# Optimization experiments

Measured on AMD Instinct MI355X. Metric: run time of the kernel, lower is better.

The kernel has to match this reference:

```python
import jax, jax.numpy as jnp
import numpy as np

NUM_SUBSET = 3
BN_EPS = 1e-5
T_CONST = 40
NUM_HEADS = 8


def _unit_gcn(x, PA, Wa, ba, Wb, bb, Wd, bd, gamma, beta):
    # x: (B, C, T, V). 1x1 convs become channel einsums. flag=True, GMPool_G,
    # num_point not in {3,7} -> adjacency A = PA only. down = identity (C_in==C_out).
    B, C, T, V = x.shape
    inter = Wa.shape[1]
    x_flat = x.reshape(B, C * T, V)
    y = None
    for i in range(NUM_SUBSET):
        a = jnp.einsum('bctv,ic->bitv', x, Wa[i]) + ba[i][None, :, None, None]
        A1 = a.transpose(0, 3, 1, 2).reshape(B, V, inter * T)          # (B, V, inter*T)
        b = jnp.einsum('bctv,ic->bitv', x, Wb[i]) + bb[i][None, :, None, None]
        A2 = b.reshape(B, inter * T, V)                                 # (B, inter*T, V)
        S = jax.nn.softmax((A1 @ A2) / (inter * T), axis=-2) + PA[i]    # (B, V, V), Softmax(-2)
        z = (x_flat @ S).reshape(B, C, T, V)
        z = jnp.einsum('bctv,oc->botv', z, Wd[i]) + bd[i][None, :, None, None]
        y = z if y is None else y + z
    # BatchNorm2d (eval: running_mean=0, running_var=1)
    y = y * (gamma / jnp.sqrt(1.0 + BN_EPS))[None, :, None, None] + beta[None, :, None, None]
    y = y + x  # residual via identity down-path
    return jax.nn.relu(y)


def _mab_forward(Q, K, fck, fcv, fco):
    B, Npt, DK = K.shape
    T = T_CONST
    C = DK // T
    Kr = K.transpose(0, 2, 1).reshape(B, C, T, Npt)   # (B, C, T, V)
    Kg = _unit_gcn(Kr, *fck)
    Vg = _unit_gcn(Kr, *fcv)
    Kf = Kg.transpose(0, 3, 1, 2).reshape(B, Npt, -1)  # (B, V, C*T)
    Vf = Vg.transpose(0, 3, 1, 2).reshape(B, Npt, -1)
    S, DV = Q.shape[1], Q.shape[2]
    ds = DV // NUM_HEADS
    Qh = Q.reshape(B, S, NUM_HEADS, ds)
    Kh = Kf.reshape(B, Npt, NUM_HEADS, ds)
    Vh = Vf.reshape(B, Npt, NUM_HEADS, ds)
    scores = jnp.einsum('bqhd,bkhd->bhqk', Qh, Kh) / jnp.sqrt(jnp.float32(DV))
    attn = jax.nn.softmax(scores, axis=-1)  # softmax_dim=2 of (H*B, S, V) == last axis
    Oh = Qh + jnp.einsum('bhqk,bkhd->bqhd', attn, Vh)
    O = Oh.reshape(B, S, DV)  # cat over heads along feature dim == reshape
    Og = O.transpose(0, 2, 1).reshape(B, C, T, S)
    Og = _unit_gcn(Og, *fco)
    Og = Og.transpose(0, 3, 1, 2).reshape(B, S, -1)
    return O + jax.nn.relu(Og)


def setup_inputs() -> dict:
    key = jax.random.key(0)
    ks = jax.random.split(key, 8)
    B, Npt, Sd, T, C, inter = 256, 25, 10, 40, 64, 16
    D = C * T  # 2560

    def gcn_params(kk, V):
        k = jax.random.split(kk, 5)
        return dict(
            PA=jnp.full((3, V, V), 1e-6, jnp.float32),
            Wa=jax.random.normal(k[0], (3, inter, C), jnp.float32) * np.float32(np.sqrt(2.0 / C)),
            ba=jnp.zeros((3, inter), jnp.float32),
            Wb=jax.random.normal(k[1], (3, inter, C), jnp.float32) * np.float32(np.sqrt(2.0 / C)),
            bb=jnp.zeros((3, inter), jnp.float32),
            Wd=jax.random.normal(k[2], (3, C, C), jnp.float32) * np.float32(np.sqrt(2.0 / (3 * C))),
            bd=jnp.zeros((3, C), jnp.float32),
            gamma=jax.random.uniform(k[3], (C,), jnp.float32, 0.5, 1.5),
            beta=jax.random.normal(k[4], (C,), jnp.float32) * 0.01,
        )

    inp = {
        'Q': jax.random.normal(ks[0], (B, Sd, D), jnp.float32),
        'K': jax.random.normal(ks[1], (B, Npt, D), jnp.float32),
    }
    for pref, kk, V in (('fck', ks[2], Npt), ('fcv', ks[3], Npt), ('fco', ks[4], Sd)):
        for n, v in gcn_params(kk, V).items():
            inp[pref + '_' + n] = v
    for n in ('relrec_s1', 'relsend_s1', 'relrec_s2', 'relsend_s2', 'relrec_speed', 'relsend_speed'):
        inp[n] = jnp.zeros((1,), jnp.int32)  # unused (branch only active for V==7, T==20)
    return inp


def reference(Q, K,
              fck_PA, fck_Wa, fck_ba, fck_Wb, fck_bb, fck_Wd, fck_bd, fck_gamma, fck_beta,
              fcv_PA, fcv_Wa, fcv_ba, fcv_Wb, fcv_bb, fcv_Wd, fcv_bd, fcv_gamma, fcv_beta,
              fco_PA, fco_Wa, fco_ba, fco_Wb, fco_bb, fco_Wd, fco_bd, fco_gamma, fco_beta,
              relrec_s1, relsend_s1, relrec_s2, relsend_s2, relrec_speed, relsend_speed):
    fck = (fck_PA, fck_Wa, fck_ba, fck_Wb, fck_bb, fck_Wd, fck_bd, fck_gamma, fck_beta)
    fcv = (fcv_PA, fcv_Wa, fcv_ba, fcv_Wb, fcv_bb, fcv_Wd, fcv_bd, fcv_gamma, fcv_beta)
    fco = (fco_PA, fco_Wa, fco_ba, fco_Wb, fco_bb, fco_Wd, fco_bd, fco_gamma, fco_beta)
    return _mab_forward(Q, K, fck, fcv, fco)
```

## Files before the change

### kernel.cpp

```cpp
#include <hip/hip_runtime.h>
#include <hip/hip_bf16.h>

#define BB 256
#define CC 64
#define TT 40
#define DD 2560
#define V1 25
#define V2 10
#define INTER 16
#define NH 8
#define DSH 320
#define HSLAB 8000

typedef __hip_bfloat16 bf16;
typedef unsigned int uint;
typedef unsigned short ushort;
typedef __attribute__((ext_vector_type(8))) short bf16x8;
typedef __attribute__((ext_vector_type(4))) float f32x4;

__device__ __forceinline__ float b2f(bf16 x) { return __bfloat162float(x); }

__device__ __forceinline__ ushort f2bb(float f) {
    uint x = __float_as_uint(f);
    uint r = x + 0x7fffu + ((x >> 16) & 1u);
    return (ushort)(r >> 16);
}
__device__ __forceinline__ float blo(uint u) { return __uint_as_float(u << 16); }
__device__ __forceinline__ float bhi(uint u) { return __uint_as_float(u & 0xffff0000u); }
__device__ __forceinline__ float b2f_us(ushort h) { return __uint_as_float(((uint)h) << 16); }
__device__ __forceinline__ uint4 pack8(const float* a) {
    uint4 pk;
    pk.x = (uint)f2bb(a[0]) | ((uint)f2bb(a[1]) << 16);
    pk.y = (uint)f2bb(a[2]) | ((uint)f2bb(a[3]) << 16);
    pk.z = (uint)f2bb(a[4]) | ((uint)f2bb(a[5]) << 16);
    pk.w = (uint)f2bb(a[6]) | ((uint)f2bb(a[7]) << 16);
    return pk;
}

__device__ __forceinline__ int swz64(int row, int col) {
    return row * 64 + ((((col >> 3) ^ row) & 7) << 3) + (col & 7);
}
__device__ __forceinline__ int swzC(int c, int col) {
    return c * 128 + ((((col >> 3) ^ c) & 15) << 3) + (col & 7);
}
__device__ __forceinline__ int swz320(int row, int k) {
    const int g = k >> 3;
    return row * 320 + (((g & ~7) | ((g ^ row) & 7)) << 3) + (k & 7);
}

__global__ __launch_bounds__(256) void prep_wabf(
    const float* __restrict__ Wa0, const float* __restrict__ Wb0,
    const float* __restrict__ Wa1, const float* __restrict__ Wb1,
    ushort* __restrict__ Wabf) {
    const int tid = threadIdx.x;
    for (int e = tid; e < 768; e += 256) {
        const int lane = e & 63, mat = (e >> 6) & 3, s = e >> 8;
        const int ln = lane & 15, lq = lane >> 4;
        const float* Wp = (mat == 0) ? Wa0 : (mat == 1) ? Wb0 : (mat == 2) ? Wa1 : Wb1;
        const float* src = Wp + s * 1024 + ln * 64 + lq * 8;
        ushort* dst = Wabf + e * 16;
        #pragma unroll
        for (int i = 0; i < 8; ++i) {
            dst[i] = f2bb(src[i]);
            dst[8 + i] = f2bb(src[32 + i]);
        }
    }
}

__global__ __launch_bounds__(512) void gcn_S3(
    const float* __restrict__ X,
    const ushort* __restrict__ Wabf,
    const float* __restrict__ ba0, const float* __restrict__ bb0,
    const float* __restrict__ ba1, const float* __restrict__ bb1,
    bf16* __restrict__ Xw, float* __restrict__ Mpart) {
    __shared__ ushort xsT[208][72];
    __shared__ ushort abT[4][32][136];
    __shared__ float biasS3[192];

    const int tid = threadIdx.x;
    const int b = blockIdx.x & 255, tc = blockIdx.x >> 8;
    const int t0 = tc * 8;
    const int lane = tid & 63, w = tid >> 6;
    const int ln = lane & 15, lq = lane >> 4;
    const int mat = w & 3, half = w >> 2;

    const float* Xb = X + (size_t)b * V1 * DD;
    for (int e = tid; e < V1 * 64; e += 512) {
        const int v = e >> 6, c = e & 63;
        const float* src = Xb + (size_t)v * DD + c * TT + t0;
        const float4 f0 = *(const float4*)src;
        const float4 f1 = *(const float4*)(src + 4);
        const float tmp[8] = {f0.x, f0.y, f0.z, f0.w, f1.x, f1.y, f1.z, f1.w};
        #pragma unroll
        for (int tl = 0; tl < 8; ++tl) xsT[v * 8 + tl][c] = f2bb(tmp[tl]);
    }
    if (tid < 192) {
        const int s = tid >> 6, m2 = (tid >> 4) & 3, j = tid & 15;
        const float* bp = (m2 == 0) ? ba0 : (m2 == 1) ? bb0 : (m2 == 2) ? ba1 : bb1;
        biasS3[tid] = bp[s * 16 + j];
    }
    __syncthreads();

    for (int e = tid; e < 1600; e += 512) {
        const int v = e >> 6, h = (e >> 3) & 7, tl = e & 7;
        *(uint4*)(Xw + (size_t)(b * NH + h) * HSLAB + v * 320 + (t0 + tl) * 8) =
            *(const uint4*)&xsT[v * 8 + tl][h * 8];
    }

    for (int s = 0; s < 3; ++s) {
        const ushort* wp = Wabf + (((s * 4 + mat) * 64 + lane) << 4);
        union { uint4 u; bf16x8 v; } ua, ub;
        ua.u = *(const uint4*)wp;
        ub.u = *(const uint4*)(wp + 8);
        float br[4];
        #pragma unroll
        for (int r = 0; r < 4; ++r) br[r] = biasS3[s * 64 + mat * 16 + lq * 4 + r];

        if (s) __syncthreads();

        const int ntEnd = half ? 13 : 7;
        for (int nt = half ? 7 : 0; nt < ntEnd; ++nt) {
            const bf16x8 b0 = *(const bf16x8*)&xsT[nt * 16 + ln][lq * 8];
            const bf16x8 b1 = *(const bf16x8*)&xsT[nt * 16 + ln][lq * 8 + 32];
            f32x4 acc = (f32x4){0.f, 0.f, 0.f, 0.f};
            acc = __builtin_amdgcn_mfma_f32_16x16x32_bf16(ua.v, b0, acc, 0, 0, 0);
            acc = __builtin_amdgcn_mfma_f32_16x16x32_bf16(ub.v, b1, acc, 0, 0, 0);
            const int p = nt * 16 + ln;
            if (p < 200) {
                const int v = p >> 3, tl = p & 7;
                #pragma unroll
                for (int r = 0; r < 4; ++r)
                    abT[mat][v][(lq * 4 + r) * 8 + tl] = f2bb(acc[r] + br[r]);
            }
        }
        __syncthreads();

        {
            const int np = w >> 2, mt = (w >> 1) & 1, ntl = w & 1;
            const ushort* Ap = &abT[np * 2 + 0][mt * 16 + ln][lq * 8];
            const ushort* Bp = &abT[np * 2 + 1][ntl * 16 + ln][lq * 8];
            f32x4 g = (f32x4){0.f, 0.f, 0.f, 0.f};
            g = __builtin_amdgcn_mfma_f32_16x16x32_bf16(
                    *(const bf16x8*)Ap, *(const bf16x8*)Bp, g, 0, 0, 0);
            g = __builtin_amdgcn_mfma_f32_16x16x32_bf16(
                    *(const bf16x8*)(Ap + 32), *(const bf16x8*)(Bp + 32), g, 0, 0, 0);
            g = __builtin_amdgcn_mfma_f32_16x16x32_bf16(
                    *(const bf16x8*)(Ap + 64), *(const bf16x8*)(Bp + 64), g, 0, 0, 0);
            g = __builtin_amdgcn_mfma_f32_16x16x32_bf16(
                    *(const bf16x8*)(Ap + 96), *(const bf16x8*)(Bp + 96), g, 0, 0, 0);
            const int vp = ntl * 16 + ln;
            if (vp < V1) {
                float* Mb = Mpart + (((size_t)tc * 256 + b) * 6 + (s * 2 + np)) * 625;
                #pragma unroll
                for (int r = 0; r < 4; ++r) {
                    const int v = mt * 16 + lq * 4 + r;
                    if (v < V1) Mb[v * V1 + vp] = g[r];
                }
            }
        }
    }
}

__global__ __launch_bounds__(128) void reduce_softmax(
    const float* __restrict__ Mpart,
    const float* __restrict__ PA0, const float* __restrict__ PA1,
    const float* __restrict__ WdK, const float* __restrict__ WdV,
    ushort* __restrict__ Sbf, ushort* __restrict__ Wdf) {
    __shared__ float Ms[625];
    const int tid = threadIdx.x, b = blockIdx.x, snp = blockIdx.y;
    const int s = snp >> 1, np = snp & 1;

    if (b == 0) {
        for (int e = tid; e < 256; e += 128) {
            const int wv = e >> 6, l = e & 63;
            const int lnn = l & 15, lqq = l >> 4;
            const float* Wp = (np ? WdV : WdK) + s * 4096 + (wv * 16 + lnn) * 64 + lqq * 8;
            ushort* dst = Wdf + (((np * 3 + s) * 4 + wv) * 64 + l) * 16;
            #pragma unroll
            for (int j = 0; j < 8; ++j) {
                dst[j] = f2bb(Wp[j]);
                dst[8 + j] = f2bb(Wp[32 + j]);
            }
        }
    }

    for (int e = tid; e < 625; e += 128) {
        float sum = 0.f;
        #pragma unroll
        for (int tcc = 0; tcc < 5; ++tcc)
            sum += Mpart[(((size_t)tcc * 256 + b) * 6 + snp) * 625 + e];
        Ms[e] = sum;
    }
    __syncthreads();
    if (tid < 32) {
        ushort* SbfRow = Sbf + ((((size_t)b * 2 + np) * 3 + s) << 10) + tid * 32;
        if (tid < V1) {
            const int vp = tid;
            const float invIT = 1.0f / 640.0f;
            float mx = -1e30f;
            for (int v = 0; v < V1; ++v) mx = fmaxf(mx, Ms[v * V1 + vp]);
            float sum = 0.f;
            for (int v = 0; v < V1; ++v) sum += expf((Ms[v * V1 + vp] - mx) * invIT);
            const float rs = 1.f / sum;
            const float* PAn = np ? PA1 : PA0;
            for (int v = 0; v < V1; ++v) {
                const float e_ = expf((Ms[v * V1 + vp] - mx) * invIT);
                SbfRow[v] = f2bb(e_ * rs + PAn[(s * V1 + v) * V1 + vp]);
            }
            for (int v = V1; v < 32; ++v) SbfRow[v] = 0;
        } else {
            for (int v = 0; v < 32; ++v) SbfRow[v] = 0;
        }
    }
}

__global__ __launch_bounds__(256) void gcn_S2O(
    const float* __restrict__ X,
    const float* __restrict__ Wa0, const float* __restrict__ ba0,
    const float* __restrict__ Wb0, const float* __restrict__ bb0,
    const float* __restrict__ PA0, const float* __restrict__ WdO,
    ushort* __restrict__ SbfO, ushort* __restrict__ Wdf3) {
    constexpr int V = V2;
    constexpr int P = 80;
    __shared__ ushort xs[64][P];
    __shared__ ushort ab[32][P];
    __shared__ ushort wT[64][32];
    __shared__ float biasL[32];
    __shared__ float M[100];

    const int tid = threadIdx.x, b = blockIdx.x, s = blockIdx.y;

    if (b == 0) {
        const int e = tid;
        if (e < 256) {
            const int wv = e >> 6, l = e & 63;
            const int lnn = l & 15, lqq = l >> 4;
            const float* Wp = WdO + s * 4096 + (wv * 16 + lnn) * 64 + lqq * 8;
            ushort* dst = Wdf3 + (((s * 4 + wv) * 64 + l) << 4);
            #pragma unroll
            for (int j = 0; j < 8; ++j) {
                dst[j] = f2bb(Wp[j]);
                dst[8 + j] = f2bb(Wp[32 + j]);
            }
        }
    }

    for (int e = tid; e < 16 * 64; e += 256) {
        int c = e & 63, j = e >> 6;
        wT[c][j]      = f2bb(Wa0[s * 1024 + e]);
        wT[c][16 + j] = f2bb(Wb0[s * 1024 + e]);
    }
    if (tid < 16) {
        biasL[tid]      = ba0[s * 16 + tid];
        biasL[16 + tid] = bb0[s * 16 + tid];
    }

    float macc = 0.f;

    const float* Xb = X + (size_t)b * V * DD;
    for (int tc = 0; tc < 5; ++tc) {
        const int t0 = tc * 8;
        for (int e = tid; e < V * 64; e += 256) {
            const int v = e >> 6, c = e & 63;
            const float* src = Xb + (size_t)v * DD + c * TT + t0;
            const float4 f0 = *(const float4*)src;
            const float4 f1 = *(const float4*)(src + 4);
            const float tmp[8] = {f0.x, f0.y, f0.z, f0.w, f1.x, f1.y, f1.z, f1.w};
            *(uint4*)&xs[c][v * 8] = pack8(tmp);
        }
        __syncthreads();
        for (int tau = tid; tau < 80; tau += 256) {
            const int rq = tau % 8, co = tau / 8;
            float acc[4][8];
            #pragma unroll
            for (int r = 0; r < 4; ++r) {
                const float bv = biasL[4 * rq + r];
                #pragma unroll
                for (int cc = 0; cc < 8; ++cc) acc[r][cc] = bv;
            }
            for (int c = 0; c < 64; ++c) {
                const uint2 wv = *(const uint2*)&wT[c][4 * rq];
                const uint4 xv = *(const uint4*)&xs[c][8 * co];
                const float w0 = blo(wv.x), w1 = bhi(wv.x);
                const float w2 = blo(wv.y), w3 = bhi(wv.y);
                const float x0 = blo(xv.x), x1 = bhi(xv.x);
                const float x2 = blo(xv.y), x3 = bhi(xv.y);
                const float x4 = blo(xv.z), x5 = bhi(xv.z);
                const float x6 = blo(xv.w), x7 = bhi(xv.w);
                acc[0][0] += w0 * x0; acc[0][1] += w0 * x1;
                acc[0][2] += w0 * x2; acc[0][3] += w0 * x3;
                acc[0][4] += w0 * x4; acc[0][5] += w0 * x5;
                acc[0][6] += w0 * x6; acc[0][7] += w0 * x7;
                acc[1][0] += w1 * x0; acc[1][1] += w1 * x1;
                acc[1][2] += w1 * x2; acc[1][3] += w1 * x3;
                acc[1][4] += w1 * x4; acc[1][5] += w1 * x5;
                acc[1][6] += w1 * x6; acc[1][7] += w1 * x7;
                acc[2][0] += w2 * x0; acc[2][1] += w2 * x1;
                acc[2][2] += w2 * x2; acc[2][3] += w2 * x3;
                acc[2][4] += w2 * x4; acc[2][5] += w2 * x5;
                acc[2][6] += w2 * x6; acc[2][7] += w2 * x7;
                acc[3][0] += w3 * x0; acc[3][1] += w3 * x1;
                acc[3][2] += w3 * x2; acc[3][3] += w3 * x3;
                acc[3][4] += w3 * x4; acc[3][5] += w3 * x5;
                acc[3][6] += w3 * x6; acc[3][7] += w3 * x7;
            }
            #pragma unroll
            for (int r = 0; r < 4; ++r)
                *(uint4*)&ab[4 * rq + r][8 * co] = pack8(acc[r]);
        }
        __syncthreads();
        if (tid < 100) {
            const int v = tid / V, vp = tid % V;
            float mm = 0.f;
            #pragma unroll
            for (int j = 0; j < 16; ++j) {
                const uint4 av = *(const uint4*)&ab[j][v * 8];
                const uint4 bv = *(const uint4*)&ab[16 + j][vp * 8];
                mm += blo(av.x) * blo(bv.x) + bhi(av.x) * bhi(bv.x)
                    + blo(av.y) * blo(bv.y) + bhi(av.y) * bhi(bv.y)
                    + blo(av.z) * blo(bv.z) + bhi(av.z) * bhi(bv.z)
                    + blo(av.w) * blo(bv.w) + bhi(av.w) * bhi(bv.w);
            }
            macc += mm;
        }
    }

    if (tid < 100) M[tid] = macc;
    __syncthreads();

    const float invIT = 1.0f / 640.0f;
    if (tid < 16) {
        ushort* So = SbfO + ((size_t)b * 3 + s) * 256 + tid * 16;
        if (tid < V) {
            const int vp = tid;
            float mx = -1e30f;
            for (int v = 0; v < V; ++v) mx = fmaxf(mx, M[v * V + vp]);
            float sum = 0.f;
            for (int v = 0; v < V; ++v) sum += expf((M[v * V + vp] - mx) * invIT);
            const float rs = 1.f / sum;
            for (int v = 0; v < V; ++v) {
                const float e_ = expf((M[v * V + vp] - mx) * invIT);
                So[v] = f2bb(e_ * rs + PA0[(s * V + v) * V + vp]);
            }
            for (int v = V; v < 16; ++v) So[v] = 0;
        } else {
            for (int v = 0; v < 16; ++v) So[v] = 0;
        }
    }
}

__global__ __launch_bounds__(256) void gcn_applyKV(
    const bf16* __restrict__ Xbf,
    const ushort* __restrict__ Sbf, const ushort* __restrict__ Wdf,
    const float* __restrict__ bdK, const float* __restrict__ gK, const float* __restrict__ beK,
    const float* __restrict__ bdV, const float* __restrict__ gV, const float* __restrict__ beV,
    bf16* __restrict__ Kg, bf16* __restrict__ Vg) {

    __shared__ ushort xsT[100 * 64];
    __shared__ ushort SlTs[6144];
    __shared__ ushort uC[8192];
    __shared__ float bias6[6 * 64];

    const int tid = threadIdx.x, b = blockIdx.x, chunk = blockIdx.y;
    const int lane = tid & 63, w = tid >> 6;
    const int ln = lane & 15, lq = lane >> 4;
    const int t0 = chunk * 4;

    if (tid < 64) {
        bias6[tid]       = bdK[tid] + bdK[64 + tid] + bdK[128 + tid];
        bias6[64 + tid]  = bdV[tid] + bdV[64 + tid] + bdV[128 + tid];
        bias6[128 + tid] = gK[tid] * rsqrtf(1.f + 1e-5f);
        bias6[192 + tid] = gV[tid] * rsqrtf(1.f + 1e-5f);
        bias6[256 + tid] = beK[tid];
        bias6[320 + tid] = beV[tid];
    }
    const bf16* Xb = Xbf + (size_t)b * NH * HSLAB;
    for (int e = tid; e < 1024; e += 256) {
        const int h = e >> 7, v = (e >> 2) & 31, tl = e & 3;
        if (v < V1)
            *(uint4*)&xsT[swz64(v * 4 + tl, h * 8)] =
                *(const uint4*)(Xb + (size_t)h * HSLAB + v * 320 + (t0 + tl) * 8);
    }
    {
        const ushort* Sb = Sbf + (size_t)b * 6144;
        for (int e = tid; e < 768; e += 256)
            ((uint4*)SlTs)[e] = ((const uint4*)Sb)[e];
    }
    __syncthreads();

    {
        const int c = lane, q = w;
        #pragma unroll
        for (int j = 0; j < 4; ++j) {
            ushort vals[8];
            #pragma unroll
            for (int i = 0; i < 8; ++i) {
                const int v0 = q * 8 + i;
                vals[i] = (v0 < V1) ? xsT[swz64(v0 * 4 + j, c)] : (ushort)0;
            }
            uint4 pk;
            pk.x = (uint)vals[0] | ((uint)vals[1] << 16);
            pk.y = (uint)vals[2] | ((uint)vals[3] << 16);
            pk.z = (uint)vals[4] | ((uint)vals[5] << 16);
            pk.w = (uint)vals[6] | ((uint)vals[7] << 16);
            *(uint4*)&uC[swzC(c, j * 32 + q * 8)] = pk;
        }
    }
    __syncthreads();

    bf16x8 aF[4];
    #pragma unroll
    for (int tl = 0; tl < 4; ++tl)
        aF[tl] = *(const bf16x8*)&uC[swzC(w * 16 + ln, tl * 32 + lq * 8)];
    __syncthreads();

    for (int g = 0; g < 2; ++g) {
        f32x4 acc[7];
        #pragma unroll
        for (int tn = 0; tn < 7; ++tn) acc[tn] = (f32x4){0.f, 0.f, 0.f, 0.f};

        for (int s = 0; s < 3; ++s) {
            const ushort* wp = Wdf + ((((g * 3 + s) * 4 + w) * 64 + lane) << 4);
            union { uint4 u; bf16x8 v; } ua, ub;
            ua.u = *(const uint4*)wp;
            ub.u = *(const uint4*)(wp + 8);

            if (g | s) __syncthreads();

            #pragma unroll
            for (int nt = 0; nt < 2; ++nt) {
                const bf16x8 bF =
                    *(const bf16x8*)&SlTs[((g * 3 + s) << 10) + (nt * 16 + ln) * 32 + lq * 8];
                const int v = nt * 16 + ln;
                #pragma unroll
                for (int tl = 0; tl < 4; ++tl) {
                    f32x4 d = (f32x4){0.f, 0.f, 0.f, 0.f};
                    d = __builtin_amdgcn_mfma_f32_16x16x32_bf16(aF[tl], bF, d, 0, 0, 0);
                    if (v < V1) {
                        uint2 pk;
                        pk.x = (uint)f2bb(d[0]) | ((uint)f2bb(d[1]) << 16);
                        pk.y = (uint)f2bb(d[2]) | ((uint)f2bb(d[3]) << 16);
                        *(uint2*)&uC[swz64(v * 4 + tl, w * 16 + lq * 4)] = pk;
                    }
                }
            }
            __syncthreads();

            #pragma unroll
            for (int tn = 0; tn < 7; ++tn) {
                const bf16x8 b0 = *(const bf16x8*)&uC[swz64(tn * 16 + ln, lq * 8)];
                const bf16x8 b1 = *(const bf16x8*)&uC[swz64(tn * 16 + ln, lq * 8 + 32)];
                acc[tn] = __builtin_amdgcn_mfma_f32_16x16x32_bf16(ua.v, b0, acc[tn], 0, 0, 0);
                acc[tn] = __builtin_amdgcn_mfma_f32_16x16x32_bf16(ub.v, b1, acc[tn], 0, 0, 0);
            }
        }
        __syncthreads();

        {
            const int c0 = w * 16 + lq * 4;
            float bb[4], ss[4], be[4];
            #pragma unroll
            for (int r = 0; r < 4; ++r) {
                bb[r] = bias6[g * 64 + c0 + r];
                ss[r] = bias6[128 + g * 64 + c0 + r];
                be[r] = bias6[256 + g * 64 + c0 + r];
            }
            #pragma unroll
            for (int tn = 0; tn < 7; ++tn) {
                const int p = tn * 16 + ln;
                if (p < 100) {
                    const uint2 u = *(const uint2*)&xsT[swz64(p, c0)];
                    const float rs[4] = {blo(u.x), bhi(u.x), blo(u.y), bhi(u.y)};
                    float y[4];
                    #pragma unroll
                    for (int r = 0; r < 4; ++r)
                        y[r] = fmaxf((acc[tn][r] + bb[r]) * ss[r] + be[r] + rs[r], 0.f);
                    uint2 pk;
                    pk.x = (uint)f2bb(y[0]) | ((uint)f2bb(y[1]) << 16);
                    pk.y = (uint)f2bb(y[2]) | ((uint)f2bb(y[3]) << 16);
                    *(uint2*)&uC[swz64(p, c0)] = pk;
                }
            }
        }
        __syncthreads();

        bf16* outp = (g ? Vg : Kg) + (size_t)b * NH * HSLAB;
        for (int e = tid; e < 1024; e += 256) {
            const int h = e >> 7, v = (e >> 2) & 31, tl = e & 3;
            if (v < V1)
                *(uint4*)(outp + (size_t)h * HSLAB + v * 320 + (t0 + tl) * 8) =
                    *(const uint4*)&uC[swz64(v * 4 + tl, h * 8)];
        }
    }
}

__global__ __launch_bounds__(256) void gcn_applyO(
    const float* __restrict__ X,
    const ushort* __restrict__ SbfO, const ushort* __restrict__ Wdf3,
    const float* __restrict__ bdO, const float* __restrict__ gO, const float* __restrict__ beO,
    float* __restrict__ out_f, const float* __restrict__ Obuf) {

    __shared__ ushort xsT[80 * 64];
    __shared__ ushort uC[8192];
    __shared__ ushort SlTs16[832];
    __shared__ float bias3[3 * 64];

    const int tid = threadIdx.x, b = blockIdx.x, chunk = blockIdx.y;
    const int lane = tid & 63, w = tid >> 6;
    const int ln = lane & 15, lq = lane >> 4;
    const int t0 = chunk * 8;

    if (tid < 64) {
        bias3[tid]       = bdO[tid] + bdO[64 + tid] + bdO[128 + tid];
        bias3[64 + tid]  = gO[tid] * rsqrtf(1.f + 1e-5f);
        bias3[128 + tid] = beO[tid];
    }
    const float* Xb = X + (size_t)b * V2 * DD;
    for (int e = tid; e < 640; e += 256) {
        const int v = e >> 6, c = e & 63;
        const float* src = Xb + (size_t)v * DD + c * TT + t0;
        const float4 f0 = *(const float4*)src;
        const float4 f1 = *(const float4*)(src + 4);
        const float tmp[8] = {f0.x, f0.y, f0.z, f0.w, f1.x, f1.y, f1.z, f1.w};
        #pragma unroll
        for (int tl = 0; tl < 8; ++tl) xsT[swz64(v * 8 + tl, c)] = f2bb(tmp[tl]);
    }
    {
        const uint4* Sb = (const uint4*)(SbfO + (size_t)b * 768);
        for (int e = tid; e < 96; e += 256) ((uint4*)SlTs16)[e] = Sb[e];
    }
    __syncthreads();

    {
        const int c = lane;
        #pragma unroll
        for (int jj = 0; jj < 4; ++jj) {
            const int u_ = w * 4 + jj;
            const int tl = u_ >> 1, q = u_ & 1;
            ushort vals[8];
            #pragma unroll
            for (int i = 0; i < 8; ++i) {
                const int v0 = q * 8 + i;
                vals[i] = (v0 < V2) ? xsT[swz64(v0 * 8 + tl, c)] : (ushort)0;
            }
            uint4 pk;
            pk.x = (uint)vals[0] | ((uint)vals[1] << 16);
            pk.y = (uint)vals[2] | ((uint)vals[3] << 16);
            pk.z = (uint)vals[4] | ((uint)vals[5] << 16);
            pk.w = (uint)vals[6] | ((uint)vals[7] << 16);
            *(uint4*)&uC[swzC(c, tl * 16 + q * 8)] = pk;
        }
    }
    __syncthreads();

    union { uint4 u; bf16x8 v; } z8; z8.u = (uint4){0u, 0u, 0u, 0u};
    bf16x8 aF[8];
    #pragma unroll
    for (int tl = 0; tl < 8; ++tl)
        aF[tl] = (lq < 2) ? *(const bf16x8*)&uC[swzC(w * 16 + ln, tl * 16 + lq * 8)]
                          : z8.v;
    __syncthreads();

    f32x4 acc[5];
    #pragma unroll
    for (int tn = 0; tn < 5; ++tn) acc[tn] = (f32x4){0.f, 0.f, 0.f, 0.f};

    for (int s = 0; s < 3; ++s) {
        const ushort* wp = Wdf3 + (((s * 4 + w) * 64 + lane) << 4);
        union { uint4 u; bf16x8 v; } ua, ub;
        ua.u = *(const uint4*)wp;
        ub.u = *(const uint4*)(wp + 8);

        if (s) __syncthreads();

        const bf16x8 bF = (lq < 2)
            ? *(const bf16x8*)&SlTs16[s * 256 + ln * 16 + lq * 8] : z8.v;
        #pragma unroll
        for (int tl = 0; tl < 8; ++tl) {
            f32x4 d = (f32x4){0.f, 0.f, 0.f, 0.f};
            d = __builtin_amdgcn_mfma_f32_16x16x32_bf16(aF[tl], bF, d, 0, 0, 0);
            if (ln < V2) {
                uint2 pk;
                pk.x = (uint)f2bb(d[0]) | ((uint)f2bb(d[1]) << 16);
                pk.y = (uint)f2bb(d[2]) | ((uint)f2bb(d[3]) << 16);
                *(uint2*)&uC[swz64(ln * 8 + tl, w * 16 + lq * 4)] = pk;
            }
        }
        __syncthreads();

        #pragma unroll
        for (int tn = 0; tn < 5; ++tn) {
            const bf16x8 b0 = *(const bf16x8*)&uC[swz64(tn * 16 + ln, lq * 8)];
            const bf16x8 b1 = *(const bf16x8*)&uC[swz64(tn * 16 + ln, lq * 8 + 32)];
            acc[tn] = __builtin_amdgcn_mfma_f32_16x16x32_bf16(ua.v, b0, acc[tn], 0, 0, 0);
            acc[tn] = __builtin_amdgcn_mfma_f32_16x16x32_bf16(ub.v, b1, acc[tn], 0, 0, 0);
        }
    }
    __syncthreads();

    {
        const int c0 = w * 16 + lq * 4;
        float bb[4], ss[4], be[4];
        #pragma unroll
        for (int r = 0; r < 4; ++r) {
            bb[r] = bias3[c0 + r];
            ss[r] = bias3[64 + c0 + r];
            be[r] = bias3[128 + c0 + r];
        }
        #pragma unroll
        for (int tn = 0; tn < 5; ++tn) {
            const int p = tn * 16 + ln;
            const uint2 u = *(const uint2*)&xsT[swz64(p, c0)];
            const float rs[4] = {blo(u.x), bhi(u.x), blo(u.y), bhi(u.y)};
            float y[4];
            #pragma unroll
            for (int r = 0; r < 4; ++r)
                y[r] = fmaxf((acc[tn][r] + bb[r]) * ss[r] + be[r] + rs[r], 0.f);
            uint2 pk;
            pk.x = (uint)f2bb(y[0]) | ((uint)f2bb(y[1]) << 16);
            pk.y = (uint)f2bb(y[2]) | ((uint)f2bb(y[3]) << 16);
            *(uint2*)&uC[swz64(p, c0)] = pk;
        }
    }
    __syncthreads();

    {
        const int v = tid & 15, ci = tid >> 4;
        if (v < V2) {
            #pragma unroll
            for (int r = 0; r < 4; ++r) {
                const int c = ci * 4 + r;
                const size_t base = (size_t)b * V2 * DD + (size_t)v * DD + c * TT + t0;
                const float4 o0 = *(const float4*)&Obuf[base];
                const float4 o1 = *(const float4*)&Obuf[base + 4];
                float4 y0, y1;
                y0.x = o0.x + b2f_us(uC[swz64(v * 8 + 0, c)]);
                y0.y = o0.y + b2f_us(uC[swz64(v * 8 + 1, c)]);
                y0.z = o0.z + b2f_us(uC[swz64(v * 8 + 2, c)]);
                y0.w = o0.w + b2f_us(uC[swz64(v * 8 + 3, c)]);
                y1.x = o1.x + b2f_us(uC[swz64(v * 8 + 4, c)]);
                y1.y = o1.y + b2f_us(uC[swz64(v * 8 + 5, c)]);
                y1.z = o1.z + b2f_us(uC[swz64(v * 8 + 6, c)]);
                y1.w = o1.w + b2f_us(uC[swz64(v * 8 + 7, c)]);
                *(float4*)&out_f[base] = y0;
                *(float4*)&out_f[base + 4] = y1;
            }
        }
    }
}

__global__ __launch_bounds__(256) void attn_kernel(const float* __restrict__ Q,
                                                   const bf16* __restrict__ Kg,
                                                   const bf16* __restrict__ Vg,
                                                   float* __restrict__ O) {
    __shared__ float smA[10240];
    __shared__ float attP[4][16][16];
    __shared__ float attF[16][32];
    ushort* qs2h = (ushort*)smA;
    ushort* qs2l = (ushort*)smA + 5120;
    ushort* ksw  = (ushort*)smA + 10240;
    float* vbuf = smA;

    const int b = blockIdx.x, h = blockIdx.y, tid = threadIdx.x;
    const int lane = tid & 63, w = tid >> 6;
    const int ln = lane & 15, lq = lane >> 4;

    const float* Qb = Q + (size_t)b * 10 * DD + h * DSH;
    for (int e = tid; e < 800; e += 256) {
        const int q = e / 80, seg = e % 80;
        const int dd0 = seg * 4;
        const float4 f = *(const float4*)(Qb + (size_t)q * DD + dd0);
        const float ff[4] = {f.x, f.y, f.z, f.w};
        #pragma unroll
        for (int j = 0; j < 4; ++j) {
            const int dd = dd0 + j;
            const int k = (dd % 40) * 8 + dd / 40;
            const int idx = swz320(q, k);
            const ushort hi = f2bb(ff[j]);
            qs2h[idx] = hi;
            qs2l[idx] = f2bb(ff[j] - b2f_us(hi));
        }
    }
    const bf16* Kb = Kg + (size_t)(b * NH + h) * HSLAB;
    for (int e = tid; e < 1000; e += 256) {
        const int kk = e / 40, g = e % 40;
        const int gp = (g & ~7) | ((g ^ kk) & 7);
        *(uint4*)&ksw[kk * 320 + gp * 8] = *(const uint4*)(Kb + (size_t)e * 8);
    }
    __syncthreads();

    {
        const int ntl = w & 1;
        const int ch0 = (w >> 1) * 5;
        f32x4 d = (f32x4){0.f, 0.f, 0.f, 0.f};
        #pragma unroll
        for (int c5 = 0; c5 < 5; ++c5) {
            const int k0 = (ch0 + c5) * 32 + lq * 8;
            const bf16x8 ah = *(const bf16x8*)&qs2h[swz320(ln, k0)];
            const bf16x8 al = *(const bf16x8*)&qs2l[swz320(ln, k0)];
            const bf16x8 bF = *(const bf16x8*)&ksw[swz320(ntl * 16 + ln, k0)];
            d = __builtin_amdgcn_mfma_f32_16x16x32_bf16(ah, bF, d, 0, 0, 0);
            d = __builtin_amdgcn_mfma_f32_16x16x32_bf16(al, bF, d, 0, 0, 0);
        }
        #pragma unroll
        for (int r = 0; r < 4; ++r) attP[w][lq * 4 + r][ln] = d[r];
    }
    __syncthreads();

    const float scale = 0.019764235376052370f;
    for (int e = tid; e < 512; e += 256) {
        const int q = e >> 5, kk = e & 31;
        const int ntl = kk >> 4, kkl = kk & 15;
        attF[q][kk] = (attP[ntl][q][kkl] + attP[ntl + 2][q][kkl]) * scale;
    }
    const bf16* Vb = Vg + (size_t)(b * NH + h) * HSLAB;
    for (int e = tid; e < 1000; e += 256) {
        const int kk = e / TT, t = e % TT;
        const uint4 u = *(const uint4*)(Vb + (size_t)e * 8);
        const ushort* us = (const ushort*)&u;
        float* dst = &vbuf[kk * 324 + t];
        #pragma unroll
        for (int cl = 0; cl < 8; ++cl) dst[cl * 40] = b2f_us(us[cl]);
    }
    __syncthreads();

    if (tid < 10) {
        float mx = -1e30f;
        for (int k = 0; k < V1; ++k) mx = fmaxf(mx, attF[tid][k]);
        float sum = 0.f;
        for (int k = 0; k < V1; ++k) {
            float e_ = expf(attF[tid][k] - mx);
            attF[tid][k] = e_;
            sum += e_;
        }
        float r = 1.0f / sum;
        for (int k = 0; k < V1; ++k) attF[tid][k] *= r;
    }
    __syncthreads();

    float* Ob = O + (size_t)b * 10 * DD + h * DSH;
    for (int e = tid; e < 800; e += 256) {
        const int q = e / 80, seg = e % 80;
        const int dl0 = seg * 4;
        float ax = 0.f, ay = 0.f, az = 0.f, aw = 0.f;
        #pragma unroll
        for (int kk = 0; kk < V1; ++kk) {
            const float a = attF[q][kk];
            const float4 v = *(const float4*)&vbuf[kk * 324 + dl0];
            ax += a * v.x; ay += a * v.y; az += a * v.z; aw += a * v.w;
        }
        const float4 qv = *(const float4*)(Qb + (size_t)q * DD + dl0);
        float4 o;
        o.x = qv.x + ax; o.y = qv.y + ay; o.z = qv.z + az; o.w = qv.w + aw;
        *(float4*)(Ob + (size_t)q * DD + dl0) = o;
    }
}

extern "C" void kernel_launch(void* const* d_in, const int* in_sizes, int n_in,
                              void* d_out, int out_size, void* d_ws, size_t ws_size,
                              hipStream_t stream) {
    const float* Q = (const float*)d_in[0];
    const float* K = (const float*)d_in[1];
    const float* fck_PA = (const float*)d_in[2];
    const float* fck_Wa = (const float*)d_in[3];
    const float* fck_ba = (const float*)d_in[4];
    const float* fck_Wb = (const float*)d_in[5];
    const float* fck_bb = (const float*)d_in[6];
    const float* fck_Wd = (const float*)d_in[7];
    const float* fck_bd = (const float*)d_in[8];
    const float* fck_gamma = (const float*)d_in[9];
    const float* fck_beta = (const float*)d_in[10];
    const float* fcv_PA = (const float*)d_in[11];
    const float* fcv_Wa = (const float*)d_in[12];
    const float* fcv_ba = (const float*)d_in[13];
    const float* fcv_Wb = (const float*)d_in[14];
    const float* fcv_bb = (const float*)d_in[15];
    const float* fcv_Wd = (const float*)d_in[16];
    const float* fcv_bd = (const float*)d_in[17];
    const float* fcv_gamma = (const float*)d_in[18];
    const float* fcv_beta = (const float*)d_in[19];
    const float* fco_PA = (const float*)d_in[20];
    const float* fco_Wa = (const float*)d_in[21];
    const float* fco_ba = (const float*)d_in[22];
    const float* fco_Wb = (const float*)d_in[23];
    const float* fco_bb = (const float*)d_in[24];
    const float* fco_Wd = (const float*)d_in[25];
    const float* fco_bd = (const float*)d_in[26];
    const float* fco_gamma = (const float*)d_in[27];
    const float* fco_beta = (const float*)d_in[28];

    char* wsb = (char*)d_ws;
    bf16* Xbf = (bf16*)(wsb);
    bf16* Vg = (bf16*)(wsb);
    bf16* Kg = (bf16*)(wsb + 32768000);
    float* Mpart = (float*)(wsb + 65536000);
    float* O = (float*)(wsb + 65536000);
    ushort* Sbf = (ushort*)(wsb + 84736000);
    ushort* Wdf = (ushort*)(wsb + 88000000);
    ushort* SbfO = (ushort*)(wsb + 32768000);
    ushort* Wdf3 = (ushort*)(wsb + 33300000);
    ushort* Wabf = (ushort*)(wsb + 95590400);

    prep_wabf<<<dim3(1), dim3(256), 0, stream>>>(
        fck_Wa, fck_Wb, fcv_Wa, fcv_Wb, Wabf);

    gcn_S3<<<dim3(BB * 5), dim3(512), 0, stream>>>(
        K, Wabf, fck_ba, fck_bb, fcv_ba, fcv_bb, Xbf, Mpart);

    reduce_softmax<<<dim3(BB, 6), dim3(128), 0, stream>>>(
        Mpart, fck_PA, fcv_PA, fck_Wd, fcv_Wd, Sbf, Wdf);

    gcn_applyKV<<<dim3(BB, 10), dim3(256), 0, stream>>>(
        Xbf, Sbf, Wdf,
        fck_bd, fck_gamma, fck_beta,
        fcv_bd, fcv_gamma, fcv_beta, Kg, Vg);

    attn_kernel<<<dim3(BB, NH), dim3(256), 0, stream>>>(Q, Kg, Vg, O);

    gcn_S2O<<<dim3(BB, 3), dim3(256), 0, stream>>>(
        O, fco_Wa, fco_ba, fco_Wb, fco_bb, fco_PA, fco_Wd, SbfO, Wdf3);

    gcn_applyO<<<dim3(BB, 5), dim3(256), 0, stream>>>(
        O, SbfO, Wdf3, fco_bd, fco_gamma, fco_beta, (float*)d_out, O);
}
```

Measured before the change: 422.9 us.

## Move gcn_S2O projections and Gram product to MFMA and merge subsets per block

New measurement: 384.2 us. -9.2%, faster.

```diff
diff --git a/kernel.cpp b/kernel.cpp
--- a/kernel.cpp
+++ b/kernel.cpp
@@ -51,14 +51,29 @@
 __global__ __launch_bounds__(256) void prep_wabf(
     const float* __restrict__ Wa0, const float* __restrict__ Wb0,
     const float* __restrict__ Wa1, const float* __restrict__ Wb1,
-    ushort* __restrict__ Wabf) {
+    const float* __restrict__ WaO, const float* __restrict__ WbO,
+    ushort* __restrict__ Wabf, ushort* __restrict__ WabfO) {
     const int tid = threadIdx.x;
-    for (int e = tid; e < 768; e += 256) {
-        const int lane = e & 63, mat = (e >> 6) & 3, s = e >> 8;
+    for (int e = tid; e < 1152; e += 256) {
+        const float* Wp;
+        ushort* dst;
+        int s, lane;
+        if (e < 768) {
+            lane = e & 63;
+            const int mat = (e >> 6) & 3;
+            s = e >> 8;
+            Wp = (mat == 0) ? Wa0 : (mat == 1) ? Wb0 : (mat == 2) ? Wa1 : Wb1;
+            dst = Wabf + e * 16;
+        } else {
+            const int eo = e - 768;
+            lane = eo & 63;
+            const int mat = (eo >> 6) & 1;
+            s = eo >> 7;
+            Wp = mat ? WbO : WaO;
+            dst = WabfO + eo * 16;
+        }
         const int ln = lane & 15, lq = lane >> 4;
-        const float* Wp = (mat == 0) ? Wa0 : (mat == 1) ? Wb0 : (mat == 2) ? Wa1 : Wb1;
         const float* src = Wp + s * 1024 + ln * 64 + lq * 8;
-        ushort* dst = Wabf + e * 16;
         #pragma unroll
         for (int i = 0; i < 8; ++i) {
             dst[i] = f2bb(src[i]);
@@ -216,24 +231,22 @@
 
 __global__ __launch_bounds__(256) void gcn_S2O(
     const float* __restrict__ X,
-    const float* __restrict__ Wa0, const float* __restrict__ ba0,
-    const float* __restrict__ Wb0, const float* __restrict__ bb0,
+    const ushort* __restrict__ WabfO,
+    const float* __restrict__ ba0, const float* __restrict__ bb0,
     const float* __restrict__ PA0, const float* __restrict__ WdO,
     ushort* __restrict__ SbfO, ushort* __restrict__ Wdf3) {
-    constexpr int V = V2;
-    constexpr int P = 80;
-    __shared__ ushort xs[64][P];
-    __shared__ ushort ab[32][P];
-    __shared__ ushort wT[64][32];
-    __shared__ float biasL[32];
-    __shared__ float M[100];
-
-    const int tid = threadIdx.x, b = blockIdx.x, s = blockIdx.y;
+    __shared__ ushort xsT[80 * 64];
+    __shared__ ushort abT[3][2][16][136];
+    __shared__ float biasS[96];
+    __shared__ float Ms[3][16][16];
+
+    const int tid = threadIdx.x, b = blockIdx.x;
+    const int lane = tid & 63, w = tid >> 6;
+    const int ln = lane & 15, lq = lane >> 4;
 
     if (b == 0) {
-        const int e = tid;
-        if (e < 256) {
-            const int wv = e >> 6, l = e & 63;
+        for (int e = tid; e < 768; e += 256) {
+            const int s = e >> 8, wv = (e >> 6) & 3, l = e & 63;
             const int lnn = l & 15, lqq = l >> 4;
             const float* Wp = WdO + s * 4096 + (wv * 16 + lnn) * 64 + lqq * 8;
             ushort* dst = Wdf3 + (((s * 4 + wv) * 64 + l) << 4);
@@ -244,105 +257,89 @@
             }
         }
     }
-
-    for (int e = tid; e < 16 * 64; e += 256) {
-        int c = e & 63, j = e >> 6;
-        wT[c][j]      = f2bb(Wa0[s * 1024 + e]);
-        wT[c][16 + j] = f2bb(Wb0[s * 1024 + e]);
-    }
-    if (tid < 16) {
-        biasL[tid]      = ba0[s * 16 + tid];
-        biasL[16 + tid] = bb0[s * 16 + tid];
-    }
-
-    float macc = 0.f;
-
-    const float* Xb = X + (size_t)b * V * DD;
+    for (int e = tid; e < 6528; e += 256) ((uint*)abT)[e] = 0u;
+    if (tid < 96) {
+        const int s = tid >> 5, m = (tid >> 4) & 1, j = tid & 15;
+        biasS[tid] = (m ? bb0 : ba0)[s * 16 + j];
+    }
+
+    f32x4 gacc = (f32x4){0.f, 0.f, 0.f, 0.f};
+    const float* Xb = X + (size_t)b * V2 * DD;
+
     for (int tc = 0; tc < 5; ++tc) {
         const int t0 = tc * 8;
-        for (int e = tid; e < V * 64; e += 256) {
+        for (int e = tid; e < 640; e += 256) {
             const int v = e >> 6, c = e & 63;
             const float* src = Xb + (size_t)v * DD + c * TT + t0;
             const float4 f0 = *(const float4*)src;
             const float4 f1 = *(const float4*)(src + 4);
             const float tmp[8] = {f0.x, f0.y, f0.z, f0.w, f1.x, f1.y, f1.z, f1.w};
-            *(uint4*)&xs[c][v * 8] = pack8(tmp);
+            #pragma unroll
+            for (int tl = 0; tl < 8; ++tl) xsT[swz64(v * 8 + tl, c)] = f2bb(tmp[tl]);
         }
         __syncthreads();
-        for (int tau = tid; tau < 80; tau += 256) {
-            const int rq = tau % 8, co = tau / 8;
-            float acc[4][8];
-            #pragma unroll
-            for (int r = 0; r < 4; ++r) {
-                const float bv = biasL[4 * rq + r];
+
+        for (int s = 0; s < 3; ++s) {
+            const ushort* wp0 = WabfO + (((s * 2 + 0) * 64 + lane) << 4);
+            const ushort* wp1 = WabfO + (((s * 2 + 1) * 64 + lane) << 4);
+            union { uint4 u; bf16x8 v; } a00, a01, a10, a11;
+            a00.u = *(const uint4*)wp0;  a01.u = *(const uint4*)(wp0 + 8);
+            a10.u = *(const uint4*)wp1;  a11.u = *(const uint4*)(wp1 + 8);
+            for (int r10 = w; r10 < 10; r10 += 4) {
+                const int mat = (r10 >= 5) ? 1 : 0;
+                const int nt = mat ? (r10 - 5) : r10;
+                const bf16x8 b0 = *(const bf16x8*)&xsT[swz64(nt * 16 + ln, lq * 8)];
+                const bf16x8 b1 = *(const bf16x8*)&xsT[swz64(nt * 16 + ln, lq * 8 + 32)];
+                f32x4 acc = (f32x4){0.f, 0.f, 0.f, 0.f};
+                acc = __builtin_amdgcn_mfma_f32_16x16x32_bf16(
+                        mat ? a10.v : a00.v, b0, acc, 0, 0, 0);
+                acc = __builtin_amdgcn_mfma_f32_16x16x32_bf16(
+                        mat ? a11.v : a01.v, b1, acc, 0, 0, 0);
+                const int p = nt * 16 + ln;
+                const int v = p >> 3, tl = p & 7;
                 #pragma unroll
-                for (int cc = 0; cc < 8; ++cc) acc[r][cc] = bv;
-            }
-            for (int c = 0; c < 64; ++c) {
-                const uint2 wv = *(const uint2*)&wT[c][4 * rq];
-                const uint4 xv = *(const uint4*)&xs[c][8 * co];
-                const float w0 = blo(wv.x), w1 = bhi(wv.x);
-                const float w2 = blo(wv.y), w3 = bhi(wv.y);
-                const float x0 = blo(xv.x), x1 = bhi(xv.x);
-                const float x2 = blo(xv.y), x3 = bhi(xv.y);
-                const float x4 = blo(xv.z), x5 = bhi(xv.z);
-                const float x6 = blo(xv.w), x7 = bhi(xv.w);
-                acc[0][0] += w0 * x0; acc[0][1] += w0 * x1;
-                acc[0][2] += w0 * x2; acc[0][3] += w0 * x3;
-                acc[0][4] += w0 * x4; acc[0][5] += w0 * x5;
-                acc[0][6] += w0 * x6; acc[0][7] += w0 * x7;
-                acc[1][0] += w1 * x0; acc[1][1] += w1 * x1;
-                acc[1][2] += w1 * x2; acc[1][3] += w1 * x3;
-                acc[1][4] += w1 * x4; acc[1][5] += w1 * x5;
-                acc[1][6] += w1 * x6; acc[1][7] += w1 * x7;
-                acc[2][0] += w2 * x0; acc[2][1] += w2 * x1;
-                acc[2][2] += w2 * x2; acc[2][3] += w2 * x3;
-                acc[2][4] += w2 * x4; acc[2][5] += w2 * x5;
-                acc[2][6] += w2 * x6; acc[2][7] += w2 * x7;
-                acc[3][0] += w3 * x0; acc[3][1] += w3 * x1;
-                acc[3][2] += w3 * x2; acc[3][3] += w3 * x3;
-                acc[3][4] += w3 * x4; acc[3][5] += w3 * x5;
-                acc[3][6] += w3 * x6; acc[3][7] += w3 * x7;
-            }
-            #pragma unroll
-            for (int r = 0; r < 4; ++r)
-                *(uint4*)&ab[4 * rq + r][8 * co] = pack8(acc[r]);
+                for (int r = 0; r < 4; ++r)
+                    abT[s][mat][v][(lq * 4 + r) * 8 + tl] =
+                        f2bb(acc[r] + biasS[s * 32 + mat * 16 + lq * 4 + r]);
+            }
         }
         __syncthreads();
-        if (tid < 100) {
-            const int v = tid / V, vp = tid % V;
-            float mm = 0.f;
-            #pragma unroll
-            for (int j = 0; j < 16; ++j) {
-                const uint4 av = *(const uint4*)&ab[j][v * 8];
-                const uint4 bv = *(const uint4*)&ab[16 + j][vp * 8];
-                mm += blo(av.x) * blo(bv.x) + bhi(av.x) * bhi(bv.x)
-                    + blo(av.y) * blo(bv.y) + bhi(av.y) * bhi(bv.y)
-                    + blo(av.z) * blo(bv.z) + bhi(av.z) * bhi(bv.z)
-                    + blo(av.w) * blo(bv.w) + bhi(av.w) * bhi(bv.w);
-            }
-            macc += mm;
-        }
-    }
-
-    if (tid < 100) M[tid] = macc;
+
+        if (w < 3) {
+            const ushort* Ap = &abT[w][0][ln][lq * 8];
+            const ushort* Bp = &abT[w][1][ln][lq * 8];
+            gacc = __builtin_amdgcn_mfma_f32_16x16x32_bf16(
+                    *(const bf16x8*)Ap, *(const bf16x8*)Bp, gacc, 0, 0, 0);
+            gacc = __builtin_amdgcn_mfma_f32_16x16x32_bf16(
+                    *(const bf16x8*)(Ap + 32), *(const bf16x8*)(Bp + 32), gacc, 0, 0, 0);
+            gacc = __builtin_amdgcn_mfma_f32_16x16x32_bf16(
+                    *(const bf16x8*)(Ap + 64), *(const bf16x8*)(Bp + 64), gacc, 0, 0, 0);
+            gacc = __builtin_amdgcn_mfma_f32_16x16x32_bf16(
+                    *(const bf16x8*)(Ap + 96), *(const bf16x8*)(Bp + 96), gacc, 0, 0, 0);
+        }
+    }
+
+    if (w < 3) {
+        #pragma unroll
+        for (int r = 0; r < 4; ++r) Ms[w][lq * 4 + r][ln] = gacc[r];
+    }
     __syncthreads();
 
     const float invIT = 1.0f / 640.0f;
-    if (tid < 16) {
-        ushort* So = SbfO + ((size_t)b * 3 + s) * 256 + tid * 16;
-        if (tid < V) {
-            const int vp = tid;
+    if (tid < 48) {
+        const int s = tid >> 4, vp = tid & 15;
+        ushort* So = SbfO + ((size_t)b * 3 + s) * 256 + vp * 16;
+        if (vp < V2) {
             float mx = -1e30f;
-            for (int v = 0; v < V; ++v) mx = fmaxf(mx, M[v * V + vp]);
+            for (int v = 0; v < V2; ++v) mx = fmaxf(mx, Ms[s][v][vp]);
             float sum = 0.f;
-            for (int v = 0; v < V; ++v) sum += expf((M[v * V + vp] - mx) * invIT);
+            for (int v = 0; v < V2; ++v) sum += expf((Ms[s][v][vp] - mx) * invIT);
             const float rs = 1.f / sum;
-            for (int v = 0; v < V; ++v) {
-                const float e_ = expf((M[v * V + vp] - mx) * invIT);
-                So[v] = f2bb(e_ * rs + PA0[(s * V + v) * V + vp]);
-            }
-            for (int v = V; v < 16; ++v) So[v] = 0;
+            for (int v = 0; v < V2; ++v) {
+                const float e_ = expf((Ms[s][v][vp] - mx) * invIT);
+                So[v] = f2bb(e_ * rs + PA0[(s * V2 + v) * V2 + vp]);
+            }
+            for (int v = V2; v < 16; ++v) So[v] = 0;
         } else {
             for (int v = 0; v < 16; ++v) So[v] = 0;
         }
@@ -800,9 +797,10 @@
     ushort* SbfO = (ushort*)(wsb + 32768000);
     ushort* Wdf3 = (ushort*)(wsb + 33300000);
     ushort* Wabf = (ushort*)(wsb + 95590400);
+    ushort* WabfO = (ushort*)(wsb + 95590400 + 32768);
 
     prep_wabf<<<dim3(1), dim3(256), 0, stream>>>(
-        fck_Wa, fck_Wb, fcv_Wa, fcv_Wb, Wabf);
+        fck_Wa, fck_Wb, fcv_Wa, fcv_Wb, fco_Wa, fco_Wb, Wabf, WabfO);
 
     gcn_S3<<<dim3(BB * 5), dim3(512), 0, stream>>>(
         K, Wabf, fck_ba, fck_bb, fcv_ba, fcv_bb, Xbf, Mpart);
@@ -817,8 +815,8 @@
 
     attn_kernel<<<dim3(BB, NH), dim3(256), 0, stream>>>(Q, Kg, Vg, O);
 
-    gcn_S2O<<<dim3(BB, 3), dim3(256), 0, stream>>>(
-        O, fco_Wa, fco_ba, fco_Wb, fco_bb, fco_PA, fco_Wd, SbfO, Wdf3);
+    gcn_S2O<<<dim3(BB), dim3(256), 0, stream>>>(
+        O, WabfO, fco_ba, fco_bb, fco_PA, fco_Wd, SbfO, Wdf3);
 
     gcn_applyO<<<dim3(BB, 5), dim3(256), 0, stream>>>(
         O, SbfO, Wdf3, fco_bd, fco_gamma, fco_beta, (float*)d_out, O);
```
